# Performance work log

Measured on AMD Instinct MI355X. Metric: run time of the kernel, lower is better.

## Reference

```python
import jax, jax.numpy as jnp
import numpy as np

# Dimensions (Llama-3-8B-style GQA with paged KV cache)
B, S, HID = 1, 1024, 4096
H, HKV, D = 32, 8, 128
G = H // HKV
BLK = 16            # tokens per KV block
NB = 256            # blocks in storage
CB = 192            # context blocks attended (3072 tokens)
PAST = 2048         # tokens already cached before this step
NL = 2              # layers in kv_ptr
L = CB * BLK


def rotate_half(x):
    x1, x2 = x[..., : x.shape[-1] // 2], x[..., x.shape[-1] // 2:]
    return jnp.concatenate([-x2, x1], axis=-1)


def setup_inputs() -> dict:
    key = jax.random.key(0)
    ks = jax.random.split(key, 8)
    hidden_states = jax.random.normal(ks[0], (B, S, HID), jnp.float32)
    kv_ptr = jax.random.normal(ks[1], (NL, 2, NB, HKV, BLK, D), jnp.float32)
    Wq = 0.02 * jax.random.normal(ks[2], (H * D, HID), jnp.float32)
    Wk = 0.02 * jax.random.normal(ks[3], (HKV * D, HID), jnp.float32)
    Wv = 0.02 * jax.random.normal(ks[4], (HKV * D, HID), jnp.float32)
    Wo = 0.02 * jax.random.normal(ks[5], (HID, H * D), jnp.float32)
    # RoPE cache for the new tokens (global positions PAST..PAST+S-1), HF convention
    pos = (PAST + jnp.arange(S)).astype(jnp.float32)
    inv_freq = 1.0 / (10000.0 ** (jnp.arange(0, D, 2, dtype=jnp.float32) / D))
    freqs = pos[:, None] * inv_freq[None, :]                # [S, D/2]
    emb = jnp.concatenate([freqs, freqs], axis=-1)           # [S, D]
    cos = jnp.cos(emb)[None, None]                           # [1,1,S,D]
    sin = jnp.sin(emb)[None, None]
    new_q_lut = jnp.arange(S, dtype=jnp.int32)[None]         # identity query LUT
    new_kv_lut = (CB - S // BLK + jnp.arange(S // BLK, dtype=jnp.int32))[None]  # blocks 128..191
    all_kv_lut = jnp.arange(CB, dtype=jnp.int32)[None]       # blocks 0..191
    kv_pos = jnp.arange(L)
    q_pos = PAST + jnp.arange(S)
    mask = (kv_pos[None, None, :] <= q_pos[None, :, None])   # [1,S,L] causal over global positions
    cmd_groups = jnp.zeros((B, S), jnp.int32)                # split-K scheduling metadata (no math effect)
    return dict(hidden_states=hidden_states, kv_ptr=kv_ptr, new_q_lut=new_q_lut,
                new_kv_lut=new_kv_lut, all_kv_lut=all_kv_lut, mask=mask,
                cmd_groups=cmd_groups, cos=cos, sin=sin, Wq=Wq, Wk=Wk, Wv=Wv, Wo=Wo,
                layer_idx=0)


def reference(hidden_states, kv_ptr, new_q_lut, new_kv_lut, all_kv_lut, mask,
              cmd_groups, cos, sin, Wq, Wk, Wv, Wo, layer_idx):
    b, s, _ = hidden_states.shape
    # QKV projections (no bias)
    q = jnp.einsum('bsh,oh->bso', hidden_states, Wq).reshape(b, s, H, D).transpose(0, 2, 1, 3)
    k = jnp.einsum('bsh,oh->bso', hidden_states, Wk).reshape(b, s, HKV, D).transpose(0, 2, 1, 3)
    v = jnp.einsum('bsh,oh->bso', hidden_states, Wv).reshape(b, s, HKV, D).transpose(0, 2, 1, 3)
    # RoPE
    q = q * cos + rotate_half(q) * sin
    k = k * cos + rotate_half(k) * sin
    # fill_kv_block_storage: scatter new K/V blocks into this layer's storage (b == 1)
    kb = jnp.transpose(k[0].reshape(HKV, s // BLK, BLK, D), (1, 0, 2, 3))  # [nblk,HKV,BLK,D]
    vb = jnp.transpose(v[0].reshape(HKV, s // BLK, BLK, D), (1, 0, 2, 3))
    sk = kv_ptr[layer_idx, 0].at[new_kv_lut[0]].set(kb)
    sv = kv_ptr[layer_idx, 1].at[new_kv_lut[0]].set(vb)
    # qkv_attention: gather context blocks via LUT, masked GQA attention
    ck = jnp.transpose(sk[all_kv_lut[0]], (1, 0, 2, 3)).reshape(HKV, L, D)  # [HKV,L,D]
    cv = jnp.transpose(sv[all_kv_lut[0]], (1, 0, 2, 3)).reshape(HKV, L, D)
    qg = q[:, :, new_q_lut[0], :].reshape(b, HKV, G, s, D)
    scores = jnp.einsum('bkgsd,kld->bkgsl', qg, ck) / jnp.sqrt(jnp.float32(D))
    scores = jnp.where(mask[:, None, None], scores, jnp.finfo(scores.dtype).min)
    p = jax.nn.softmax(scores, axis=-1)
    o = jnp.einsum('bkgsl,kld->bkgsd', p, cv).reshape(b, H, s, D)
    o = o.transpose(0, 2, 1, 3).reshape(b, s, H * D)
    return jnp.einsum('bso,ho->bsh', o, Wo)
```

## Files before the change

### kernel.cpp

```cpp
#include <hip/hip_runtime.h>
#include <cstdint>
#include <cstddef>


typedef _Float16 f16;
typedef f16 f16x8 __attribute__((ext_vector_type(8)));
typedef f16 f16x4 __attribute__((ext_vector_type(4)));
typedef float f32x4 __attribute__((ext_vector_type(4)));

#define HIDN 4096
#define LCTX 3072
#define PASTN 2048
#define QK_SCALE_LOG2 0.12753102734366334f
#define RESC_THR 11.54f

__device__ __forceinline__ f32x4 mfma16(f16x8 a, f16x8 b, f32x4 c) {
    return __builtin_amdgcn_mfma_f32_16x16x32_f16(a, b, c, 0, 0, 0);
}
__device__ __forceinline__ f32x4 mfma16k16(f16x4 a, f16x4 b, f32x4 c) {
    return __builtin_amdgcn_mfma_f32_16x16x16f16(a, b, c, 0, 0, 0);
}

__device__ __forceinline__ void gl_lds16(const void* g, void* l) {
    auto gp = (const __attribute__((address_space(1))) unsigned int*)(uintptr_t)g;
    auto lp = (__attribute__((address_space(3))) unsigned int*)(uintptr_t)l;
    __builtin_amdgcn_global_load_lds(gp, lp, 16, 0, 0);
}

__device__ __forceinline__ uint32_t lds_lo(const void* p) {
    return (uint32_t)(uintptr_t)p;
}

#define TRRD(dst, va, OFF) \
    asm volatile("ds_read_b64_tr_b16 %0, %1 offset:" #OFF : "=v"(dst) : "v"(va))
#define WAITL(N) \
    asm volatile("s_waitcnt lgkmcnt(" #N ")" ::: "memory"); \
    __builtin_amdgcn_sched_barrier(0)

__global__ void cvt_all(const float* __restrict__ hidden, const float* __restrict__ Wq,
                        const float* __restrict__ Wk, const float* __restrict__ Wv,
                        f16* __restrict__ h16, f16* __restrict__ w16)
{
    int i = blockIdx.x * 256 + threadIdx.x;
    const float* src; f16* dst; int off;
    if (i < 1048576)      { src = hidden; dst = h16; off = i; }
    else if (i < 5242880) { src = Wq; dst = w16; off = i - 1048576; }
    else if (i < 6291456) { src = Wk; dst = w16 + (size_t)4096 * 4096; off = i - 5242880; }
    else                  { src = Wv; dst = w16 + (size_t)5120 * 4096; off = i - 6291456; }
    f32x4 v = *(const f32x4*)(src + (size_t)off * 4);
    f16x4 h;
#pragma unroll
    for (int j = 0; j < 4; j++) h[j] = (f16)v[j];
    *(f16x4*)(dst + (size_t)off * 4) = h;
}

__global__ void cvt_f32_f16(const float* __restrict__ src, f16* __restrict__ dst, int n4)
{
    int i = blockIdx.x * 256 + threadIdx.x;
    if (i >= n4) return;
    f32x4 v = *(const f32x4*)(src + (size_t)i * 4);
    f16x4 h;
#pragma unroll
    for (int j = 0; j < 4; j++) h[j] = (f16)v[j];
    *(f16x4*)(dst + (size_t)i * 4) = h;
}

template <int EPI>
__global__ __launch_bounds__(256, 3) void gemm_f16(
    const f16* __restrict__ A, const f16* __restrict__ B,
    float* __restrict__ Cf, f16* __restrict__ Cq, f16* __restrict__ Ck,
    f16* __restrict__ Cv, int M, int N, int K)
{
    __shared__ f16 As[128 * 64];
    __shared__ f16 Bs[128 * 64];

    const int t = threadIdx.x, lane = t & 63, w = t >> 6;
    const int wm = w >> 1, wn = w & 1;
    const int l16 = lane & 15, g16 = lane >> 4;
    const int m0 = blockIdx.y * 128, n0 = blockIdx.x * 128;

    const int srow = lane >> 3;
    const int sgr  = (lane & 7) ^ srow;

    const size_t aoff = (size_t)(m0 + w * 32 + srow) * K + sgr * 8;
    const size_t boff = (size_t)(n0 + w * 32 + srow) * K + sgr * 8;

    f32x4 acc[4][4];
#pragma unroll
    for (int i = 0; i < 4; i++)
#pragma unroll
        for (int j = 0; j < 4; j++) acc[i][j] = (f32x4){0.f, 0.f, 0.f, 0.f};

    for (int k0 = 0; k0 < K; k0 += 64) {
#pragma unroll
        for (int j = 0; j < 4; j++) {
            gl_lds16(A + aoff + (size_t)j * 8 * K + k0, (void*)(As + (w * 32 + j * 8) * 64));
            gl_lds16(B + boff + (size_t)j * 8 * K + k0, (void*)(Bs + (w * 32 + j * 8) * 64));
        }
        __syncthreads();

#pragma unroll
        for (int ks = 0; ks < 2; ks++) {
            f16x8 af[4], bfr[4];
#pragma unroll
            for (int mi = 0; mi < 4; mi++) {
                int r = wm * 64 + mi * 16 + l16;
                int g = ks * 4 + g16;
                af[mi] = *(const f16x8*)&As[r * 64 + ((g ^ (r & 7)) << 3)];
            }
#pragma unroll
            for (int ni = 0; ni < 4; ni++) {
                int r = wn * 64 + ni * 16 + l16;
                int g = ks * 4 + g16;
                bfr[ni] = *(const f16x8*)&Bs[r * 64 + ((g ^ (r & 7)) << 3)];
            }
#pragma unroll
            for (int ni = 0; ni < 4; ni++)
#pragma unroll
                for (int mi = 0; mi < 4; mi++)
                    acc[mi][ni] = mfma16(af[mi], bfr[ni], acc[mi][ni]);
        }
        __syncthreads();
    }

#pragma unroll
    for (int mi = 0; mi < 4; mi++)
#pragma unroll
        for (int ni = 0; ni < 4; ni++)
#pragma unroll
            for (int r = 0; r < 4; r++) {
                int row = m0 + wm * 64 + mi * 16 + (g16 << 2) + r;
                int col = n0 + wn * 64 + ni * 16 + l16;
                float val = acc[mi][ni][r];
                if (EPI == 0) {
                    if (col < 4096) {
                        Cq[(size_t)row * 4096 + col] = (f16)val;
                    } else if (col < 5120) {
                        Ck[(size_t)row * 1024 + (col - 4096)] = (f16)val;
                    } else {
                        int c = col - 5120;
                        int hh = c >> 7, d = c & 127;
                        Cv[((size_t)hh * LCTX + PASTN + row) * 128 + d] = (f16)val;
                    }
                } else {
                    Cf[(size_t)row * N + col] = val;
                }
            }
}

__global__ void rope_q(f16* __restrict__ q, const float* __restrict__ cosp,
                       const float* __restrict__ sinp)
{
    int i = blockIdx.x * 256 + threadIdx.x;
    int gd = i & 7, hh = (i >> 3) & 31, s = i >> 8;
    size_t b1 = (size_t)s * 4096 + hh * 128 + gd * 8;
    f16x8 x1 = *(f16x8*)(q + b1);
    f16x8 x2 = *(f16x8*)(q + b1 + 64);
    const float* c1 = cosp + s * 128 + gd * 8;
    const float* s1 = sinp + s * 128 + gd * 8;
    const float* c2 = c1 + 64;
    const float* s2 = s1 + 64;
    f16x8 o1, o2;
#pragma unroll
    for (int j = 0; j < 8; j++) {
        float a = (float)x1[j], b = (float)x2[j];
        o1[j] = (f16)((a * c1[j] - b * s1[j]) * QK_SCALE_LOG2);
        o2[j] = (f16)((b * c2[j] + a * s2[j]) * QK_SCALE_LOG2);
    }
    *(f16x8*)(q + b1) = o1;
    *(f16x8*)(q + b1 + 64) = o2;
}

__global__ void rope_k(const f16* __restrict__ kraw, const float* __restrict__ cosp,
                       const float* __restrict__ sinp, f16* __restrict__ ck)
{
    int i = blockIdx.x * 256 + threadIdx.x;
    int gd = i & 7, kvh = (i >> 3) & 7, s = i >> 6;
    size_t b1 = (size_t)s * 1024 + kvh * 128 + gd * 8;
    f16x8 x1 = *(const f16x8*)(kraw + b1);
    f16x8 x2 = *(const f16x8*)(kraw + b1 + 64);
    const float* c1 = cosp + s * 128 + gd * 8;
    const float* s1 = sinp + s * 128 + gd * 8;
    const float* c2 = c1 + 64;
    const float* s2 = s1 + 64;
    f16x8 o1, o2;
#pragma unroll
    for (int j = 0; j < 8; j++) {
        float a = (float)x1[j], b = (float)x2[j];
        o1[j] = (f16)(a * c1[j] - b * s1[j]);
        o2[j] = (f16)(b * c2[j] + a * s2[j]);
    }
    size_t dst = ((size_t)kvh * LCTX + PASTN + s) * 128 + gd * 8;
    *(f16x8*)(ck + dst) = o1;
    *(f16x8*)(ck + dst + 64) = o2;
}

__global__ void cache_conv(const float* __restrict__ kvp, const int* __restrict__ layer,
                           f16* __restrict__ ck, f16* __restrict__ cv)
{
    int i4 = blockIdx.x * 256 + threadIdx.x;
    int half = i4 >> 19;
    int e = (i4 & 524287) * 4;
    int hh = e >> 18, rem = e & 262143, l = rem >> 7, d = rem & 127;
    int blk = l >> 4, rr = l & 15;
    size_t src = (((size_t)(layer[0] * 2 + half) * 256 + blk) * 8 + hh) * 2048
               + (size_t)rr * 128 + d;
    f32x4 x = *(const f32x4*)(kvp + src);
    f16x4 h;
#pragma unroll
    for (int j = 0; j < 4; j++) h[j] = (f16)x[j];
    size_t dst = ((size_t)hh * LCTX + l) * 128 + d;
    *(f16x4*)((half ? cv : ck) + dst) = h;
}

__global__ __launch_bounds__(256, 2) void attn_f16(
    const f16* __restrict__ Q, const f16* __restrict__ Kc,
    const f16* __restrict__ Vc, f16* __restrict__ Og)
{
    const int b = blockIdx.x;
    const int idx = b & 255;
    const int h = idx & 31;
    const int jt = idx >> 5;
    const int tile = (b >> 8) ? (15 - jt) : jt;
    const int s0 = tile * 64;
    const int kvh = h >> 2;
    const int t = threadIdx.x, lane = t & 63, w = t >> 6;
    const int l16 = lane & 15, g16 = lane >> 4;

    __shared__ f16 Ks[2][64 * 128];
    __shared__ f16 Vs[2][64 * 128];

    f16x8 qf[4];
    {
        size_t base = (size_t)(s0 + w * 16 + l16) * 4096 + h * 128;
#pragma unroll
        for (int kk = 0; kk < 4; kk++)
            qf[kk] = *(const f16x8*)(Q + base + kk * 32 + g16 * 8);
    }

    f32x4 of[8];
#pragma unroll
    for (int cf = 0; cf < 8; cf++) of[cf] = (f32x4){0.f, 0.f, 0.f, 0.f};
    float mr = -3.0e38f, lr = 0.f;

    const f16* Kb = Kc + (size_t)kvh * LCTX * 128;
    const f16* Vb = Vc + (size_t)kvh * LCTX * 128;
    const int nt = (PASTN + s0 + 64) >> 6;

    const int krow = lane >> 4;
    const int kp   = lane & 15;
    const int vrow = ((lane >> 5) << 4) + (((lane >> 3) & 3) << 2) + ((lane >> 1) & 3);
    const int vch  = (lane & 1) << 3;

    const uint32_t vs0 = lds_lo(Vs[0]) + lane * 8;
    const uint32_t vs1 = lds_lo(Vs[1]) + lane * 8;

#define STAGE_KV(l0, buf)                                                     \
    {                                                                         \
        _Pragma("unroll")                                                     \
        for (int j = 0; j < 4; j++) {                                         \
            int r7 = ((j & 1) << 2) + krow;                                   \
            int sg = kp ^ r7;                                                 \
            gl_lds16(Kb + (size_t)((l0) + w * 16 + j * 4 + krow) * 128 + sg * 8, \
                     (void*)(Ks[buf] + (w * 16 + j * 4) * 128));              \
        }                                                                     \
        _Pragma("unroll")                                                     \
        for (int q = 0; q < 4; q++) {                                         \
            gl_lds16(Vb + (size_t)((l0) + (q & 1) * 32 + vrow) * 128          \
                        + (w * 2 + (q >> 1)) * 16 + vch,                      \
                     (void*)(Vs[buf] + (w * 4 + q) * 512));                   \
        }                                                                     \
    }

    STAGE_KV(0, 0);
    __syncthreads();

    for (int it = 0; it < nt; ++it) {
        const int l0 = it << 6;
        const int cur = it & 1;

        if (it + 1 < nt) STAGE_KV(l0 + 64, cur ^ 1);

        f32x4 sf[4];
#pragma unroll
        for (int ni = 0; ni < 4; ni++) sf[ni] = (f32x4){0.f, 0.f, 0.f, 0.f};
        __builtin_amdgcn_s_setprio(1);
#pragma unroll
        for (int ni = 0; ni < 4; ni++)
#pragma unroll
            for (int kk = 0; kk < 4; kk++) {
                int r = ni * 16 + l16;
                int g = kk * 4 + g16;
                f16x8 kh = *(const f16x8*)&Ks[cur][r * 128 + ((g ^ (r & 7)) << 3)];
                sf[ni] = mfma16(kh, qf[kk], sf[ni]);
            }
        __builtin_amdgcn_s_setprio(0);

        const int qrow = s0 + w * 16 + l16;
        const bool needmask = (l0 + 63 > PASTN + s0);
        if (needmask) {
#pragma unroll
            for (int ni = 0; ni < 4; ni++)
#pragma unroll
                for (int r = 0; r < 4; r++) {
                    int col = l0 + ni * 16 + (g16 << 2) + r;
                    if (col > PASTN + qrow) sf[ni][r] = -3.0e38f;
                }
        }

        float mx;
        {
            f32x4 m4 = sf[0];
#pragma unroll
            for (int ni = 1; ni < 4; ni++) {
                m4[0] = fmaxf(m4[0], sf[ni][0]); m4[1] = fmaxf(m4[1], sf[ni][1]);
                m4[2] = fmaxf(m4[2], sf[ni][2]); m4[3] = fmaxf(m4[3], sf[ni][3]);
            }
            mx = fmaxf(fmaxf(m4[0], m4[1]), fmaxf(m4[2], m4[3]));
        }
        mx = fmaxf(mx, __shfl_xor(mx, 16));
        mx = fmaxf(mx, __shfl_xor(mx, 32));
        if (__any(mx > mr + RESC_THR)) {
            float mnew = fmaxf(mr, mx);
            float corr = exp2f(mr - mnew);
            mr = mnew;
            lr *= corr;
            float cr[4];
#pragma unroll
            for (int r = 0; r < 4; r++) cr[r] = __shfl(corr, (g16 << 2) + r);
#pragma unroll
            for (int cf = 0; cf < 8; cf++)
#pragma unroll
                for (int r = 0; r < 4; r++) of[cf][r] *= cr[r];
        }
#pragma unroll
        for (int ni = 0; ni < 4; ni++)
#pragma unroll
            for (int r = 0; r < 4; r++) {
                float p = exp2f(sf[ni][r] - mr);
                sf[ni][r] = p;
                lr += p;
            }

        f16x4 pa[4];
#pragma unroll
        for (int ni = 0; ni < 4; ni++) {
            pa[ni][0] = (f16)sf[ni][0]; pa[ni][1] = (f16)sf[ni][1];
            pa[ni][2] = (f16)sf[ni][2]; pa[ni][3] = (f16)sf[ni][3];
        }

        {
            const uint32_t va = cur ? vs1 : vs0;
            f16x4 r0,r1,r2,r3,r4,r5,r6,r7,r8,r9,r10,r11,r12,r13,r14,r15,
                  r16,r17,r18,r19,r20,r21,r22,r23,r24,r25,r26,r27,r28,r29,r30,r31;
            __builtin_amdgcn_s_setprio(1);
            TRRD(r0,va,0);      TRRD(r1,va,512);    TRRD(r2,va,1024);   TRRD(r3,va,1536);
            TRRD(r4,va,2048);   TRRD(r5,va,2560);   TRRD(r6,va,3072);   TRRD(r7,va,3584);
            TRRD(r8,va,4096);   TRRD(r9,va,4608);   TRRD(r10,va,5120);  TRRD(r11,va,5632);
#define X16(cf, ni, reg) of[cf] = mfma16k16(pa[ni], reg, of[cf]);
            WAITL(8);
            X16(0,0,r0)  X16(0,1,r1)  X16(0,2,r2)  X16(0,3,r3)
            TRRD(r12,va,6144);  TRRD(r13,va,6656);  TRRD(r14,va,7168);  TRRD(r15,va,7680);
            WAITL(8);
            X16(1,0,r4)  X16(1,1,r5)  X16(1,2,r6)  X16(1,3,r7)
            TRRD(r16,va,8192);  TRRD(r17,va,8704);  TRRD(r18,va,9216);  TRRD(r19,va,9728);
            WAITL(8);
            X16(2,0,r8)  X16(2,1,r9)  X16(2,2,r10) X16(2,3,r11)
            TRRD(r20,va,10240); TRRD(r21,va,10752); TRRD(r22,va,11264); TRRD(r23,va,11776);
            WAITL(8);
            X16(3,0,r12) X16(3,1,r13) X16(3,2,r14) X16(3,3,r15)
            TRRD(r24,va,12288); TRRD(r25,va,12800); TRRD(r26,va,13312); TRRD(r27,va,13824);
            WAITL(8);
            X16(4,0,r16) X16(4,1,r17) X16(4,2,r18) X16(4,3,r19)
            TRRD(r28,va,14336); TRRD(r29,va,14848); TRRD(r30,va,15360); TRRD(r31,va,15872);
            WAITL(8);
            X16(5,0,r20) X16(5,1,r21) X16(5,2,r22) X16(5,3,r23)
            WAITL(4);
            X16(6,0,r24) X16(6,1,r25) X16(6,2,r26) X16(6,3,r27)
            WAITL(0);
            X16(7,0,r28) X16(7,1,r29) X16(7,2,r30) X16(7,3,r31)
#undef X16
            __builtin_amdgcn_s_setprio(0);
        }
        __syncthreads();
    }

    lr += __shfl_xor(lr, 16);
    lr += __shfl_xor(lr, 32);
    float lrr[4];
#pragma unroll
    for (int r = 0; r < 4; r++) lrr[r] = __shfl(lr, (g16 << 2) + r);
#pragma unroll
    for (int cf = 0; cf < 8; cf++)
#pragma unroll
        for (int r = 0; r < 4; r++) {
            int srow = s0 + w * 16 + (g16 << 2) + r;
            int d = cf * 16 + l16;
            Og[(size_t)srow * 4096 + (size_t)h * 128 + d] = (f16)(of[cf][r] / lrr[r]);
        }
#undef STAGE_KV
}

extern "C" void kernel_launch(void* const* d_in, const int* in_sizes, int n_in,
                              void* d_out, int out_size, void* d_ws, size_t ws_size,
                              hipStream_t stream)
{
    const float* hidden = (const float*)d_in[0];
    const float* kvp    = (const float*)d_in[1];
    const float* cosp   = (const float*)d_in[7];
    const float* sinp   = (const float*)d_in[8];
    const float* Wq     = (const float*)d_in[9];
    const float* Wk     = (const float*)d_in[10];
    const float* Wv     = (const float*)d_in[11];
    const float* Wo     = (const float*)d_in[12];
    const int*   layer  = (const int*)d_in[13];

    char* ws = (char*)d_ws;
    f16* w16  = (f16*)ws;
    f16* h16  = (f16*)(ws + 50331648);
    f16* ck   = (f16*)(ws + 58720256);
    f16* cv   = (f16*)(ws + 65011712);
    f16* obuf = (f16*)(ws + 71303168);

    f16* q16  = (f16*)d_out;
    f16* kraw = (f16*)((char*)d_out + 8388608);

    cvt_all<<<28672, 256, 0, stream>>>(hidden, Wq, Wk, Wv, h16, w16);

    gemm_f16<0><<<dim3(48, 8), 256, 0, stream>>>(
        h16, w16, nullptr, q16, kraw, cv, 1024, 6144, 4096);

    cvt_f32_f16<<<16384, 256, 0, stream>>>(Wo, w16, 4194304);

    rope_q<<<1024, 256, 0, stream>>>(q16, cosp, sinp);
    rope_k<<<256, 256, 0, stream>>>(kraw, cosp, sinp, ck);
    cache_conv<<<4096, 256, 0, stream>>>(kvp, layer, ck, cv);

    attn_f16<<<dim3(512), 256, 0, stream>>>(q16, ck, cv, obuf);

    gemm_f16<1><<<dim3(32, 8), 256, 0, stream>>>(
        obuf, w16, (float*)d_out, nullptr, nullptr, nullptr, 1024, 4096, 4096);
}
```

Measured before the change: 277.6 us.

## Fuse auxiliary conversion/RoPE kernels and load K directly into registers in attention

```diff
diff --git a/kernel.cpp b/kernel.cpp
--- a/kernel.cpp
+++ b/kernel.cpp
@@ -54,15 +54,69 @@
     *(f16x4*)(dst + (size_t)off * 4) = h;
 }
 
-__global__ void cvt_f32_f16(const float* __restrict__ src, f16* __restrict__ dst, int n4)
+__global__ void aux_all(const float* __restrict__ Wo, f16* __restrict__ w16,
+                        f16* __restrict__ q16, const f16* __restrict__ kraw,
+                        const float* __restrict__ cosp, const float* __restrict__ sinp,
+                        f16* __restrict__ ck, const float* __restrict__ kvp,
+                        const int* __restrict__ layer, f16* __restrict__ cv)
 {
     int i = blockIdx.x * 256 + threadIdx.x;
-    if (i >= n4) return;
-    f32x4 v = *(const f32x4*)(src + (size_t)i * 4);
-    f16x4 h;
-#pragma unroll
-    for (int j = 0; j < 4; j++) h[j] = (f16)v[j];
-    *(f16x4*)(dst + (size_t)i * 4) = h;
+    if (i < 4194304) {
+        f32x4 v = *(const f32x4*)(Wo + (size_t)i * 4);
+        f16x4 h;
+#pragma unroll
+        for (int j = 0; j < 4; j++) h[j] = (f16)v[j];
+        *(f16x4*)(w16 + (size_t)i * 4) = h;
+    } else if (i < 4456448) {
+        int ii = i - 4194304;
+        int gd = ii & 7, hh = (ii >> 3) & 31, s = ii >> 8;
+        size_t b1 = (size_t)s * 4096 + hh * 128 + gd * 8;
+        f16x8 x1 = *(f16x8*)(q16 + b1);
+        f16x8 x2 = *(f16x8*)(q16 + b1 + 64);
+        const float* c1 = cosp + s * 128 + gd * 8;
+        const float* s1 = sinp + s * 128 + gd * 8;
+        f16x8 o1, o2;
+#pragma unroll
+        for (int j = 0; j < 8; j++) {
+            float a = (float)x1[j], b = (float)x2[j];
+            o1[j] = (f16)((a * c1[j] - b * s1[j]) * QK_SCALE_LOG2);
+            o2[j] = (f16)((b * c1[j + 64] + a * s1[j + 64]) * QK_SCALE_LOG2);
+        }
+        *(f16x8*)(q16 + b1) = o1;
+        *(f16x8*)(q16 + b1 + 64) = o2;
+    } else if (i < 4521984) {
+        int ii = i - 4456448;
+        int gd = ii & 7, kvh = (ii >> 3) & 7, s = ii >> 6;
+        size_t b1 = (size_t)s * 1024 + kvh * 128 + gd * 8;
+        f16x8 x1 = *(const f16x8*)(kraw + b1);
+        f16x8 x2 = *(const f16x8*)(kraw + b1 + 64);
+        const float* c1 = cosp + s * 128 + gd * 8;
+        const float* s1 = sinp + s * 128 + gd * 8;
+        f16x8 o1, o2;
+#pragma unroll
+        for (int j = 0; j < 8; j++) {
+            float a = (float)x1[j], b = (float)x2[j];
+            o1[j] = (f16)(a * c1[j] - b * s1[j]);
+            o2[j] = (f16)(b * c1[j + 64] + a * s1[j + 64]);
+        }
+        size_t dst = ((size_t)kvh * LCTX + PASTN + s) * 128 + gd * 8;
+        *(f16x8*)(ck + dst) = o1;
+        *(f16x8*)(ck + dst + 64) = o2;
+    } else {
+        int i4 = i - 4521984;
+        int half = i4 >> 19;
+        int e = (i4 & 524287) * 4;
+        int hh = e >> 18, rem = e & 262143, l = rem >> 7, d = rem & 127;
+        int blk = l >> 4, rr = l & 15;
+        size_t src = (((size_t)(layer[0] * 2 + half) * 256 + blk) * 8 + hh) * 2048
+                   + (size_t)rr * 128 + d;
+        f32x4 x = *(const f32x4*)(kvp + src);
+        f16x4 h;
+#pragma unroll
+        for (int j = 0; j < 4; j++) h[j] = (f16)x[j];
+        size_t dst = ((size_t)hh * LCTX + l) * 128 + d;
+        *(f16x4*)((half ? cv : ck) + dst) = h;
+    }
 }
 
 template <int EPI>
@@ -148,71 +202,6 @@
             }
 }
 
-__global__ void rope_q(f16* __restrict__ q, const float* __restrict__ cosp,
-                       const float* __restrict__ sinp)
-{
-    int i = blockIdx.x * 256 + threadIdx.x;
-    int gd = i & 7, hh = (i >> 3) & 31, s = i >> 8;
-    size_t b1 = (size_t)s * 4096 + hh * 128 + gd * 8;
-    f16x8 x1 = *(f16x8*)(q + b1);
-    f16x8 x2 = *(f16x8*)(q + b1 + 64);
-    const float* c1 = cosp + s * 128 + gd * 8;
-    const float* s1 = sinp + s * 128 + gd * 8;
-    const float* c2 = c1 + 64;
-    const float* s2 = s1 + 64;
-    f16x8 o1, o2;
-#pragma unroll
-    for (int j = 0; j < 8; j++) {
-        float a = (float)x1[j], b = (float)x2[j];
-        o1[j] = (f16)((a * c1[j] - b * s1[j]) * QK_SCALE_LOG2);
-        o2[j] = (f16)((b * c2[j] + a * s2[j]) * QK_SCALE_LOG2);
-    }
-    *(f16x8*)(q + b1) = o1;
-    *(f16x8*)(q + b1 + 64) = o2;
-}
-
-__global__ void rope_k(const f16* __restrict__ kraw, const float* __restrict__ cosp,
-                       const float* __restrict__ sinp, f16* __restrict__ ck)
-{
-    int i = blockIdx.x * 256 + threadIdx.x;
-    int gd = i & 7, kvh = (i >> 3) & 7, s = i >> 6;
-    size_t b1 = (size_t)s * 1024 + kvh * 128 + gd * 8;
-    f16x8 x1 = *(const f16x8*)(kraw + b1);
-    f16x8 x2 = *(const f16x8*)(kraw + b1 + 64);
-    const float* c1 = cosp + s * 128 + gd * 8;
-    const float* s1 = sinp + s * 128 + gd * 8;
-    const float* c2 = c1 + 64;
-    const float* s2 = s1 + 64;
-    f16x8 o1, o2;
-#pragma unroll
-    for (int j = 0; j < 8; j++) {
-        float a = (float)x1[j], b = (float)x2[j];
-        o1[j] = (f16)(a * c1[j] - b * s1[j]);
-        o2[j] = (f16)(b * c2[j] + a * s2[j]);
-    }
-    size_t dst = ((size_t)kvh * LCTX + PASTN + s) * 128 + gd * 8;
-    *(f16x8*)(ck + dst) = o1;
-    *(f16x8*)(ck + dst + 64) = o2;
-}
-
-__global__ void cache_conv(const float* __restrict__ kvp, const int* __restrict__ layer,
-                           f16* __restrict__ ck, f16* __restrict__ cv)
-{
-    int i4 = blockIdx.x * 256 + threadIdx.x;
-    int half = i4 >> 19;
-    int e = (i4 & 524287) * 4;
-    int hh = e >> 18, rem = e & 262143, l = rem >> 7, d = rem & 127;
-    int blk = l >> 4, rr = l & 15;
-    size_t src = (((size_t)(layer[0] * 2 + half) * 256 + blk) * 8 + hh) * 2048
-               + (size_t)rr * 128 + d;
-    f32x4 x = *(const f32x4*)(kvp + src);
-    f16x4 h;
-#pragma unroll
-    for (int j = 0; j < 4; j++) h[j] = (f16)x[j];
-    size_t dst = ((size_t)hh * LCTX + l) * 128 + d;
-    *(f16x4*)((half ? cv : ck) + dst) = h;
-}
-
 __global__ __launch_bounds__(256, 2) void attn_f16(
     const f16* __restrict__ Q, const f16* __restrict__ Kc,
     const f16* __restrict__ Vc, f16* __restrict__ Og)
@@ -227,7 +216,6 @@
     const int t = threadIdx.x, lane = t & 63, w = t >> 6;
     const int l16 = lane & 15, g16 = lane >> 4;
 
-    __shared__ f16 Ks[2][64 * 128];
     __shared__ f16 Vs[2][64 * 128];
 
     f16x8 qf[4];
@@ -247,23 +235,17 @@
     const f16* Vb = Vc + (size_t)kvh * LCTX * 128;
     const int nt = (PASTN + s0 + 64) >> 6;
 
-    const int krow = lane >> 4;
-    const int kp   = lane & 15;
+    const f16* kaddr = Kb + (size_t)l16 * 128 + g16 * 8;
+    f16x8 kf[4][4];
+
     const int vrow = ((lane >> 5) << 4) + (((lane >> 3) & 3) << 2) + ((lane >> 1) & 3);
     const int vch  = (lane & 1) << 3;
 
     const uint32_t vs0 = lds_lo(Vs[0]) + lane * 8;
     const uint32_t vs1 = lds_lo(Vs[1]) + lane * 8;
 
-#define STAGE_KV(l0, buf)                                                     \
+#define STAGE_V(l0, buf)                                                      \
     {                                                                         \
-        _Pragma("unroll")                                                     \
-        for (int j = 0; j < 4; j++) {                                         \
-            int r7 = ((j & 1) << 2) + krow;                                   \
-            int sg = kp ^ r7;                                                 \
-            gl_lds16(Kb + (size_t)((l0) + w * 16 + j * 4 + krow) * 128 + sg * 8, \
-                     (void*)(Ks[buf] + (w * 16 + j * 4) * 128));              \
-        }                                                                     \
         _Pragma("unroll")                                                     \
         for (int q = 0; q < 4; q++) {                                         \
             gl_lds16(Vb + (size_t)((l0) + (q & 1) * 32 + vrow) * 128          \
@@ -272,14 +254,26 @@
         }                                                                     \
     }
 
-    STAGE_KV(0, 0);
+#define LOADK(l0)                                                             \
+    {                                                                         \
+        _Pragma("unroll")                                                     \
+        for (int ni = 0; ni < 4; ni++) {                                      \
+            _Pragma("unroll")                                                 \
+            for (int kk = 0; kk < 4; kk++)                                    \
+                kf[ni][kk] = *(const f16x8*)(kaddr                            \
+                    + (size_t)((l0) + ni * 16) * 128 + kk * 32);              \
+        }                                                                     \
+    }
+
+    STAGE_V(0, 0);
+    LOADK(0);
     __syncthreads();
 
     for (int it = 0; it < nt; ++it) {
         const int l0 = it << 6;
         const int cur = it & 1;
 
-        if (it + 1 < nt) STAGE_KV(l0 + 64, cur ^ 1);
+        if (it + 1 < nt) STAGE_V(l0 + 64, cur ^ 1);
 
         f32x4 sf[4];
 #pragma unroll
@@ -288,13 +282,11 @@
 #pragma unroll
         for (int ni = 0; ni < 4; ni++)
 #pragma unroll
-            for (int kk = 0; kk < 4; kk++) {
-                int r = ni * 16 + l16;
-                int g = kk * 4 + g16;
-                f16x8 kh = *(const f16x8*)&Ks[cur][r * 128 + ((g ^ (r & 7)) << 3)];
-                sf[ni] = mfma16(kh, qf[kk], sf[ni]);
-            }
+            for (int kk = 0; kk < 4; kk++)
+                sf[ni] = mfma16(kf[ni][kk], qf[kk], sf[ni]);
         __builtin_amdgcn_s_setprio(0);
+
+        if (it + 1 < nt) LOADK(l0 + 64);
 
         const int qrow = s0 + w * 16 + l16;
         const bool needmask = (l0 + 63 > PASTN + s0);
@@ -398,7 +390,8 @@
             int d = cf * 16 + l16;
             Og[(size_t)srow * 4096 + (size_t)h * 128 + d] = (f16)(of[cf][r] / lrr[r]);
         }
-#undef STAGE_KV
+#undef STAGE_V
+#undef LOADK
 }
 
 extern "C" void kernel_launch(void* const* d_in, const int* in_sizes, int n_in,
@@ -430,11 +423,8 @@
     gemm_f16<0><<<dim3(48, 8), 256, 0, stream>>>(
         h16, w16, nullptr, q16, kraw, cv, 1024, 6144, 4096);
 
-    cvt_f32_f16<<<16384, 256, 0, stream>>>(Wo, w16, 4194304);
-
-    rope_q<<<1024, 256, 0, stream>>>(q16, cosp, sinp);
-    rope_k<<<256, 256, 0, stream>>>(kraw, cosp, sinp, ck);
-    cache_conv<<<4096, 256, 0, stream>>>(kvp, layer, ck, cv);
+    aux_all<<<21760, 256, 0, stream>>>(Wo, w16, q16, kraw, cosp, sinp,
+                                       ck, kvp, layer, cv);
 
     attn_f16<<<dim3(512), 256, 0, stream>>>(q16, ck, cv, obuf);
 
```

Measured after the change: 366.2 us. +31.9%, slower.
